# Optimization experiments

Measured on AMD Instinct MI355X. Metric: run time of the kernel, lower is better.

The kernel has to match this reference:

```python
import jax, jax.numpy as jnp
import numpy as np

BETA = 1.0
POWER_ITERS = 9
EPS = 1e-12  # F.normalize default eps


def _normalize(v):
    # L2 normalize over dim=1 of [B, N, 1], matching F.normalize(x, dim=1)
    n = jnp.linalg.norm(v, axis=1, keepdims=True)
    return v / jnp.maximum(n, EPS)


def _dominant_eigenvalue(A, x):
    # A: [B, N, N], x: [B, N, 1]
    for _ in range(POWER_ITERS):
        x = _normalize(jnp.matmul(A, x))
    Ax = jnp.matmul(A, x)[..., 0]              # [B, N]
    num = jnp.sum(Ax * x[..., 0], axis=1)      # x^T A x
    den = jnp.sum(x[..., 0] ** 2, axis=1)      # ||x||^2 (== 1 after normalize)
    return num / den, x


def setup_inputs() -> dict:
    key = jax.random.key(0)
    k1, k2 = jax.random.split(key)
    B, C, H, W = 256, 2048, 7, 7
    x = jax.random.normal(k1, (B, C, H, W), dtype=jnp.float32)
    x0 = _normalize(jax.random.normal(k2, (B, H * W, 1), dtype=jnp.float32))
    return {"x": x, "x0": x0}


def reference(x, x0):
    B, C, H, W = x.shape
    N = H * W
    Wm = x.reshape(B, C, N)
    # ATA = W^T W : [B, N, N]
    ATA = jnp.einsum('bcn,bcm->bnm', Wm, Wm)
    # first power iteration: largest eigenvalue; x0 is a no_grad constant
    largest, x1 = _dominant_eigenvalue(ATA, jax.lax.stop_gradient(x0))
    I = jnp.eye(N, dtype=ATA.dtype)
    shifted = ATA - largest[:, None, None] * I
    # second power iteration warm-started from detached x1 (torch stores last_x detached)
    tmp, _ = _dominant_eigenvalue(shifted, jax.lax.stop_gradient(x1))
    smallest = tmp + largest
    penalty = BETA * (largest / smallest - 1.0) ** 2
    return jnp.sum(penalty) / B
```

## Files before the change

### kernel.cpp

```cpp
#include <hip/hip_runtime.h>
#include <hip/hip_bf16.h>
#include <stdint.h>


#define BATCH 256
#define CDIM  2048
#define NDIM  49
#define QK    512
#define CHUNK 64
#define NCHUNK (QK / CHUNK)
#define CH_FLOATS (CHUNK * NDIM)
#define CH_SLOTS  (CH_FLOATS / 4)
#define TN    56
#define NSLICE (8 * TN)
#define TILE_BYTES (8 * TN * 8 * 2)
#define RAW_BYTES (2 * CH_FLOATS * 4)
#define PSIZE (NDIM * NDIM)
#define ESTR  65
#define ASTR  53

typedef __bf16 bf16x8 __attribute__((ext_vector_type(8)));
typedef float  f32x16 __attribute__((ext_vector_type(16)));

__device__ inline void async_load16(const float* g, float* l) {
  __builtin_amdgcn_global_load_lds(
      (const __attribute__((address_space(1))) void*)g,
      (__attribute__((address_space(3))) void*)l,
      16 , 0 , 0 );
}

__global__ __launch_bounds__(256, 4) void gram_kernel(
    const float* __restrict__ x, float* __restrict__ partial,
    float* __restrict__ out) {
  __shared__ __align__(16) char smem[RAW_BYTES + 2 * TILE_BYTES];
  float*  raw0 = (float*)smem;
  float*  raw1 = (float*)(smem + CH_FLOATS * 4);
  __bf16* tH   = (__bf16*)(smem + RAW_BYTES);
  __bf16* tL   = (__bf16*)(smem + RAW_BYTES + TILE_BYTES);
  float*  Ebuf = (float*)smem;

  const int tid   = threadIdx.x;
  const int bidx  = blockIdx.x;
  const int batch = bidx >> 2;
  const int q     = bidx & 3;
  const int w     = tid >> 6;
  const int lane  = tid & 63;
  const int ln    = lane & 31;
  const int hf    = lane >> 5;
  const int qm = w >> 1, qn = w & 1;
  const int rowA = min(qm * 32 + ln, TN - 1);
  const int rowB = min(qn * 32 + ln, TN - 1);
  const int nOut = qn * 32 + ln;

  if (bidx == 0 && tid == 0) out[0] = 0.f;

  const float* gbase = x + ((size_t)batch * CDIM + (size_t)q * QK) * NDIM;

  f32x16 c1, cE;
#pragma unroll
  for (int i = 0; i < 16; ++i) { c1[i] = 0.f; cE[i] = 0.f; }

  const int s1ok = (tid < NSLICE - 256);
  const int n0 = tid % TN,         g0 = tid / TN;
  const int n1 = (256 + tid) % TN, g1 = (256 + tid) / TN;

#pragma unroll
  for (int i = 0; i < 4; ++i) {
    int slot = i * 256 + tid;
    if (slot < CH_SLOTS) async_load16(gbase + slot * 4, raw0 + slot * 4);
  }

  for (int ch = 0; ch < NCHUNK; ++ch) {
    float* cur = (ch & 1) ? raw1 : raw0;
    float* nxt = (ch & 1) ? raw0 : raw1;
    __syncthreads();

    if (ch + 1 < NCHUNK) {
      const float* gch = gbase + (size_t)(ch + 1) * CH_FLOATS;
#pragma unroll
      for (int i = 0; i < 4; ++i) {
        int slot = i * 256 + tid;
        if (slot < CH_SLOTS) async_load16(gch + slot * 4, nxt + slot * 4);
      }
    }

    if (n0 < NDIM) {
      const float* rp = cur + g0 * 8 * NDIM + n0;
      bf16x8 h8, l8;
#pragma unroll
      for (int j = 0; j < 8; ++j) {
        float v = rp[j * NDIM];
        __bf16 h = (__bf16)v;
        h8[j] = h;
        l8[j] = (__bf16)(v - (float)h);
      }
      *(bf16x8*)(tH + (g0 * TN + n0) * 8) = h8;
      *(bf16x8*)(tL + (g0 * TN + n0) * 8) = l8;
    }
    if (s1ok && n1 < NDIM) {
      const float* rp = cur + g1 * 8 * NDIM + n1;
      bf16x8 h8, l8;
#pragma unroll
      for (int j = 0; j < 8; ++j) {
        float v = rp[j * NDIM];
        __bf16 h = (__bf16)v;
        h8[j] = h;
        l8[j] = (__bf16)(v - (float)h);
      }
      *(bf16x8*)(tH + (g1 * TN + n1) * 8) = h8;
      *(bf16x8*)(tL + (g1 * TN + n1) * 8) = l8;
    }
    __syncthreads();

#pragma unroll
    for (int g2 = 0; g2 < 4; ++g2) {
      const int g = g2 * 2 + hf;
      bf16x8 ah = *(const bf16x8*)(tH + (g * TN + rowA) * 8);
      bf16x8 bh;
      if (qm == qn) bh = ah;
      else          bh = *(const bf16x8*)(tH + (g * TN + rowB) * 8);
      bf16x8 bl = *(const bf16x8*)(tL + (g * TN + rowB) * 8);
      c1 = __builtin_amdgcn_mfma_f32_32x32x16_bf16(ah, bh, c1, 0, 0, 0);
      cE = __builtin_amdgcn_mfma_f32_32x32x16_bf16(ah, bl, cE, 0, 0, 0);
    }
  }

  __syncthreads();
#pragma unroll
  for (int r = 0; r < 16; ++r) {
    const int mm = qm * 32 + (r & 3) + 8 * (r >> 2) + 4 * hf;
    Ebuf[mm * ESTR + nOut] = cE[r];
  }
  __syncthreads();
  float* outp = partial + (size_t)bidx * PSIZE;
#pragma unroll
  for (int r = 0; r < 16; ++r) {
    const int mm = qm * 32 + (r & 3) + 8 * (r >> 2) + 4 * hf;
    if (mm < NDIM && nOut < NDIM)
      outp[mm * NDIM + nOut] = c1[r] + cE[r] + Ebuf[nOut * ESTR + mm];
  }
}

__global__ __launch_bounds__(64) void eigen_kernel(
    const float* __restrict__ partial, const float* __restrict__ x0,
    float* __restrict__ out) {
  __shared__ float A[NDIM * ASTR];
  __shared__ float xv[64];

  const int b = blockIdx.x;
  const int t = threadIdx.x;
  const float* p0 = partial + (size_t)(4 * b) * PSIZE;

  for (int idx = t; idx < NDIM * NDIM; idx += 64) {
    int r = idx / NDIM;
    int c = idx - r * NDIM;
    float v = 0.f;
#pragma unroll
    for (int qq = 0; qq < 4; ++qq) v += p0[qq * PSIZE + idx];
    A[r * ASTR + c] = v;
  }
  if (t < NDIM) xv[t] = x0[b * NDIM + t];
  __syncthreads();

  auto rayleigh_power = [&](float shift) -> float {
    for (int it = 0; it < 9; ++it) {
      float y = 0.f;
      if (t < NDIM) {
        const float* Ar = &A[t * ASTR];
#pragma unroll 7
        for (int k = 0; k < NDIM; ++k) y = fmaf(Ar[k], xv[k], y);
        y -= shift * xv[t];
      }
      float s = y * y;
#pragma unroll
      for (int o = 32; o; o >>= 1) s += __shfl_xor(s, o, 64);
      float nrm = fmaxf(sqrtf(s), 1e-12f);
      __syncthreads();
      if (t < NDIM) xv[t] = y / nrm;
      __syncthreads();
    }
    float yy = 0.f;
    if (t < NDIM) {
      const float* Ar = &A[t * ASTR];
#pragma unroll 7
      for (int k = 0; k < NDIM; ++k) yy = fmaf(Ar[k], xv[k], yy);
      yy -= shift * xv[t];
    }
    float num = (t < NDIM) ? yy * xv[t] : 0.f;
    float den = (t < NDIM) ? xv[t] * xv[t] : 0.f;
#pragma unroll
    for (int o = 32; o; o >>= 1) {
      num += __shfl_xor(num, o, 64);
      den += __shfl_xor(den, o, 64);
    }
    return num / den;
  };

  float largest = rayleigh_power(0.f);
  float tmp = rayleigh_power(largest);
  float smallest = tmp + largest;

  if (t == 0) {
    float r = largest / smallest - 1.f;
    atomicAdd(out, r * r * (1.0f / (float)BATCH));
  }
}

extern "C" void kernel_launch(void* const* d_in, const int* in_sizes, int n_in,
                              void* d_out, int out_size, void* d_ws,
                              size_t ws_size, hipStream_t stream) {
  const float* x  = (const float*)d_in[0];
  const float* x0 = (const float*)d_in[1];
  float* out = (float*)d_out;
  float* partial = (float*)d_ws;

  gram_kernel<<<1024, 256, 0, stream>>>(x, partial, out);
  eigen_kernel<<<BATCH, 64, 0, stream>>>(partial, x0, out);
}
```

Measured before the change: 179.3 us.

## Fuse gram and eigen kernels using last-block-per-batch atomic counter

Merges the Gram matrix kernel and the power-iteration kernel into one launch. The last of the four blocks finishing each batch, found with an atomic counter, sums the partials and runs the eigenvalue iterations. A global done counter lets the final block write the output. This removes one kernel launch and lets eigen work overlap with other blocks' Gram computation, but it adds a memset launch and runs the serial eigen phase inside 256-thread blocks with heavy register and shared memory use. The matvec inner loop is also vectorized with float4 reads of x.

```diff
diff --git a/kernel.cpp b/kernel.cpp
--- a/kernel.cpp
+++ b/kernel.cpp
@@ -18,6 +18,7 @@
 #define PSIZE (NDIM * NDIM)
 #define ESTR  65
 #define ASTR  53
+#define CNT_OFF (1024 * PSIZE)
 
 typedef __bf16 bf16x8 __attribute__((ext_vector_type(8)));
 typedef float  f32x16 __attribute__((ext_vector_type(16)));
@@ -29,15 +30,20 @@
       16 , 0 , 0 );
 }
 
-__global__ __launch_bounds__(256, 4) void gram_kernel(
-    const float* __restrict__ x, float* __restrict__ partial,
+__global__ __launch_bounds__(256, 4) void ofpenalty_fused(
+    const float* __restrict__ x, const float* __restrict__ x0,
+    float* __restrict__ partial, unsigned int* __restrict__ cnt,
+    float* __restrict__ acc, unsigned int* __restrict__ done,
     float* __restrict__ out) {
   __shared__ __align__(16) char smem[RAW_BYTES + 2 * TILE_BYTES];
+  __shared__ int flag;
   float*  raw0 = (float*)smem;
   float*  raw1 = (float*)(smem + CH_FLOATS * 4);
   __bf16* tH   = (__bf16*)(smem + RAW_BYTES);
   __bf16* tL   = (__bf16*)(smem + RAW_BYTES + TILE_BYTES);
   float*  Ebuf = (float*)smem;
+  float*  Aeig = (float*)smem;
+  float*  xv   = (float*)(smem + 10400);
 
   const int tid   = threadIdx.x;
   const int bidx  = blockIdx.x;
@@ -52,8 +58,6 @@
   const int rowB = min(qn * 32 + ln, TN - 1);
   const int nOut = qn * 32 + ln;
 
-  if (bidx == 0 && tid == 0) out[0] = 0.f;
-
   const float* gbase = x + ((size_t)batch * CDIM + (size_t)q * QK) * NDIM;
 
   f32x16 c1, cE;
@@ -139,36 +143,44 @@
     if (mm < NDIM && nOut < NDIM)
       outp[mm * NDIM + nOut] = c1[r] + cE[r] + Ebuf[nOut * ESTR + mm];
   }
-}
-
-__global__ __launch_bounds__(64) void eigen_kernel(
-    const float* __restrict__ partial, const float* __restrict__ x0,
-    float* __restrict__ out) {
-  __shared__ float A[NDIM * ASTR];
-  __shared__ float xv[64];
-
-  const int b = blockIdx.x;
-  const int t = threadIdx.x;
-  const float* p0 = partial + (size_t)(4 * b) * PSIZE;
-
-  for (int idx = t; idx < NDIM * NDIM; idx += 64) {
-    int r = idx / NDIM;
-    int c = idx - r * NDIM;
+
+  __threadfence();
+  __syncthreads();
+  if (tid == 0) {
+    unsigned int old = atomicAdd(&cnt[batch], 1u);
+    flag = (old == 3u) ? 1 : 0;
+  }
+  __syncthreads();
+  if (!flag) return;
+  __threadfence();
+
+  const float* p0 = partial + (size_t)(batch * 4) * PSIZE;
+  for (int idx = tid; idx < PSIZE; idx += 256) {
+    int r = idx / NDIM, c = idx - r * NDIM;
     float v = 0.f;
 #pragma unroll
     for (int qq = 0; qq < 4; ++qq) v += p0[qq * PSIZE + idx];
-    A[r * ASTR + c] = v;
-  }
-  if (t < NDIM) xv[t] = x0[b * NDIM + t];
-  __syncthreads();
-
+    Aeig[r * ASTR + c] = v;
+  }
+  if (tid < NDIM) xv[tid] = x0[batch * NDIM + tid];
+  __syncthreads();
+
+  const int t = tid;
   auto rayleigh_power = [&](float shift) -> float {
     for (int it = 0; it < 9; ++it) {
       float y = 0.f;
       if (t < NDIM) {
-        const float* Ar = &A[t * ASTR];
-#pragma unroll 7
-        for (int k = 0; k < NDIM; ++k) y = fmaf(Ar[k], xv[k], y);
+        const float* Ar = &Aeig[t * ASTR];
+        const float4* xv4 = (const float4*)xv;
+#pragma unroll
+        for (int j = 0; j < 12; ++j) {
+          float4 xq = xv4[j];
+          y = fmaf(Ar[4 * j + 0], xq.x, y);
+          y = fmaf(Ar[4 * j + 1], xq.y, y);
+          y = fmaf(Ar[4 * j + 2], xq.z, y);
+          y = fmaf(Ar[4 * j + 3], xq.w, y);
+        }
+        y = fmaf(Ar[48], xv[48], y);
         y -= shift * xv[t];
       }
       float s = y * y;
@@ -181,7 +193,7 @@
     }
     float yy = 0.f;
     if (t < NDIM) {
-      const float* Ar = &A[t * ASTR];
+      const float* Ar = &Aeig[t * ASTR];
 #pragma unroll 7
       for (int k = 0; k < NDIM; ++k) yy = fmaf(Ar[k], xv[k], yy);
       yy -= shift * xv[t];
@@ -202,7 +214,13 @@
 
   if (t == 0) {
     float r = largest / smallest - 1.f;
-    atomicAdd(out, r * r * (1.0f / (float)BATCH));
+    atomicAdd(acc, r * r * (1.0f / (float)BATCH));
+    __threadfence();
+    unsigned int od = atomicAdd(done, 1u);
+    if (od == BATCH - 1) {
+      __threadfence();
+      out[0] = atomicAdd(acc, 0.0f);
+    }
   }
 }
 
@@ -213,7 +231,10 @@
   const float* x0 = (const float*)d_in[1];
   float* out = (float*)d_out;
   float* partial = (float*)d_ws;
-
-  gram_kernel<<<1024, 256, 0, stream>>>(x, partial, out);
-  eigen_kernel<<<BATCH, 64, 0, stream>>>(partial, x0, out);
+  unsigned int* cnt  = (unsigned int*)(partial + CNT_OFF);
+  float*        acc  = (float*)(cnt + 256);
+  unsigned int* done = (unsigned int*)(cnt + 257);
+
+  hipMemsetAsync((void*)cnt, 0, 258 * sizeof(unsigned int), stream);
+  ofpenalty_fused<<<1024, 256, 0, stream>>>(x, x0, partial, cnt, acc, done, out);
 }
```

After: 334.9 us. 86.8% more time.
